# Kernel tuning notes

Hardware: AMD Instinct MI355X
Metric: run time of the kernel (lower is better)

## Reference

```python
import jax, jax.numpy as jnp
import numpy as np

N = 4096          # num_nodes
F = 64            # node_features
H = 128           # hidden_dim
NH = 4            # num_heads
HD = H // NH      # per-head dim = 32
L = 3             # num_layers
C = 7             # num_classes
EDGE_P = 0.004    # ~16 avg degree


def setup_inputs() -> dict:
    key = jax.random.key(0)
    ks = jax.random.split(key, 20)
    g = lambda k, shape, fan_in: jax.random.normal(k, shape, jnp.float32) / np.sqrt(fan_in)
    x = jax.random.normal(ks[0], (N, F), jnp.float32)
    adj = (jax.random.uniform(ks[1], (N, N)) < EDGE_P).astype(jnp.float32)
    return {
        "x": x,
        "adj": adj,
        "enc_W": g(ks[2], (F, H), F), "enc_b": jnp.zeros((H,), jnp.float32),
        "gcn_W": g(ks[3], (L, H, H), H), "gcn_b": jnp.zeros((L, H), jnp.float32),
        "attn_W": g(ks[4], (L, NH, H, HD), H), "attn_Wb": jnp.zeros((L, NH, HD), jnp.float32),
        "attn_a": g(ks[5], (L, NH, 2 * HD), 2 * HD), "attn_ab": jnp.zeros((L, NH), jnp.float32),
        "cls_W1": g(ks[6], (H, H // 2), H), "cls_b1": jnp.zeros((H // 2,), jnp.float32),
        "cls_W2": g(ks[7], (H // 2, C), H // 2), "cls_b2": jnp.zeros((C,), jnp.float32),
        "con_W1": g(ks[8], (H, H // 2), H), "con_b1": jnp.zeros((H // 2,), jnp.float32),
        "con_W2": g(ks[9], (H // 2, 1), H // 2), "con_b2": jnp.zeros((1,), jnp.float32),
    }


def _normalize_adj(adj):
    a = adj + jnp.eye(adj.shape[0], dtype=adj.dtype)
    dinv = jnp.sum(a, axis=1) ** -0.5
    return dinv[:, None] * a * dinv[None, :]


def _gcn(h, adj_norm, W, b):
    support = adj_norm @ h                      # [N,H]
    return jax.nn.relu(support @ W + b)         # dropout=0 (eval)


def _attention(h, edge_mask, W, Wb, a, ab):
    # h:[N,H], W:[NH,H,HD], a:[NH,2*HD]; per-pair score = Linear(concat(h_i,h_j))
    hh = jnp.einsum('nf,hfd->hnd', h, W) + Wb[:, None, :]     # [NH,N,HD]
    a_src, a_dst = a[:, :HD], a[:, HD:]
    s_src = jnp.einsum('hnd,hd->hn', hh, a_src)               # [NH,N]
    s_dst = jnp.einsum('hnd,hd->hn', hh, a_dst)               # [NH,N]
    scores = s_src[:, :, None] + s_dst[:, None, :] + ab[:, None, None]
    # original uses literal 0.0 (NOT -inf) for non-edges before softmax
    scores = jnp.where(edge_mask[None, :, :], scores, 0.0)    # [NH,N,N]
    probs = jax.nn.softmax(scores, axis=-1)
    out = jnp.einsum('hij,hjd->hid', probs, hh)               # [NH,N,HD]
    return out.transpose(1, 0, 2).reshape(h.shape[0], NH * HD)


def reference(x, adj, enc_W, enc_b, gcn_W, gcn_b, attn_W, attn_Wb, attn_a, attn_ab,
              cls_W1, cls_b1, cls_W2, cls_b2, con_W1, con_b1, con_W2, con_b2):
    h = jax.nn.relu(x @ enc_W + enc_b)          # node encoder (dropout=0)
    adj_norm = _normalize_adj(adj)
    edge_mask = adj > 0
    for i in range(L):
        h_gcn = _gcn(h, adj_norm, gcn_W[i], gcn_b[i])
        h_attn = _attention(h, edge_mask, attn_W[i], attn_Wb[i], attn_a[i], attn_ab[i])
        h = jax.nn.relu(h_gcn + h_attn)
    node_logits = jax.nn.relu(h @ cls_W1 + cls_b1) @ cls_W2 + cls_b2
    h_mean = jnp.mean(h, axis=0, keepdims=True)
    contagion = jax.nn.relu(h_mean @ con_W1 + con_b1) @ con_W2 + con_b2
    return (node_logits, h, contagion)
```

## Files before the change

### kernel.cpp

```cpp
#include <hip/hip_runtime.h>

typedef unsigned short u16;
typedef unsigned int u32;

#define N 4096
#define F 64
#define H 128
#define NH 4
#define HD 32
#define EMAX 64

__device__ float g_hA[N * H];
__device__ float g_hB[N * H];
__device__ float g_hhA[N * H];
__device__ float g_hhB[N * H];
__device__ u16   g_cols[N * EMAX];
__device__ int   g_deg[N];
__device__ float g_dinv[N];
__device__ float g_ssrcA[N * NH];
__device__ float g_ssrcB[N * NH];
__device__ float g_sdstA[N * NH];
__device__ float g_sdstB[N * NH];
__device__ float g_part[3][32][H];
__device__ float g_hpart[32][H];

__global__ void k_csr(const float* __restrict__ adj) {
  __shared__ int cnt;
  int row = blockIdx.x;
  if (threadIdx.x == 0) cnt = 0;
  if (row == 0) {
    float* pz = &g_part[0][0][0];
    for (int i = threadIdx.x; i < 3 * 32 * H; i += 256) pz[i] = 0.f;
    float* hz = &g_hpart[0][0];
    for (int i = threadIdx.x; i < 32 * H; i += 256) hz[i] = 0.f;
  }
  __syncthreads();
  int base = threadIdx.x * 16;
  const float4* p = reinterpret_cast<const float4*>(adj + (size_t)row * N + base);
  float4 q0 = p[0], q1 = p[1], q2 = p[2], q3 = p[3];
  float vals[16] = {q0.x, q0.y, q0.z, q0.w, q1.x, q1.y, q1.z, q1.w,
                    q2.x, q2.y, q2.z, q2.w, q3.x, q3.y, q3.z, q3.w};
#pragma unroll
  for (int t = 0; t < 16; ++t)
    if (vals[t] != 0.f) {
      int pos = atomicAdd(&cnt, 1);
      if (pos < EMAX) g_cols[row * EMAX + pos] = (u16)(base + t);
    }
  __syncthreads();
  if (threadIdx.x == 0) {
    g_deg[row] = cnt < EMAX ? cnt : EMAX;
    g_dinv[row] = 1.0f / sqrtf((float)(cnt + 1));
  }
}

__device__ __forceinline__ void agg4(int i0, int tid, const float* __restrict__ h,
                                     const float* __restrict__ hhin,
                                     const float* __restrict__ ssrc_in,
                                     const float* __restrict__ sdst_in,
                                     int l, const float* __restrict__ abv,
                                     int (&jl)[4][EMAX], float (&dv)[4][EMAX],
                                     float (&sdl)[4][EMAX * NH],
                                     float& outa0, float& outa1,
                                     float& sup0, float& sup1) {
  int c = tid & 127, rg = tid >> 7, hc = c >> 5;
  int darr[4];
#pragma unroll
  for (int r = 0; r < 4; ++r) darr[r] = g_deg[i0 + r];
#pragma unroll
  for (int r = 0; r < 4; ++r) {
    const u16* cl = g_cols + (size_t)(i0 + r) * EMAX;
    for (int e = tid; e < darr[r]; e += 256) {
      int j = cl[e];
      jl[r][e] = j;
      dv[r][e] = g_dinv[j];
    }
  }
  __syncthreads();
#pragma unroll
  for (int r = 0; r < 4; ++r)
    for (int idx = tid; idx < darr[r] * NH; idx += 256)
      sdl[r][idx] = sdst_in[jl[r][idx >> 2] * NH + (idx & 3)];
  __syncthreads();

  float sumc = 0.f;
  const float* part = &g_part[l][0][0];
#pragma unroll
  for (int s = 0; s < 32; ++s) sumc += part[s * H + c];
  float ab = abv[hc];

  float oa[2], sp[2];
#pragma unroll
  for (int rr = 0; rr < 2; ++rr) {
    int r = rg * 2 + rr;
    int i = i0 + r, dd = darr[r];
    float ssrc = ssrc_in[i * NH + hc];
    float M = -INFINITY;
    for (int e = 0; e < dd; ++e) M = fmaxf(M, sdl[r][e * NH + hc]);
    float mv = fmaxf(0.f, ssrc + ab + M);
    float em = expf(-mv);
    float base = ssrc + ab - mv;
    float aA = 0.f, aT = 0.f, aG = 0.f, S = 0.f;
    int e = 0;
    for (; e + 2 <= dd; e += 2) {
      int j0 = jl[r][e], j1 = jl[r][e + 1];
      float q0 = hhin[j0 * H + c], q1 = hhin[j1 * H + c];
      float p0 = h[j0 * H + c], p1 = h[j1 * H + c];
      float w0 = expf(base + sdl[r][e * NH + hc]);
      float w1 = expf(base + sdl[r][(e + 1) * NH + hc]);
      aA = fmaf(w0, q0, aA); aA = fmaf(w1, q1, aA);
      aT += q0 + q1;
      aG = fmaf(dv[r][e], p0, aG); aG = fmaf(dv[r][e + 1], p1, aG);
      S += w0 + w1;
    }
    for (; e < dd; ++e) {
      int j = jl[r][e];
      float w = expf(base + sdl[r][e * NH + hc]);
      float q = hhin[j * H + c];
      aA = fmaf(w, q, aA);
      aT += q;
      aG = fmaf(dv[r][e], h[j * H + c], aG);
      S += w;
    }
    float Z = S + em * (float)(N - dd);
    oa[rr] = (aA + em * (sumc - aT)) / Z;
    float di = g_dinv[i];
    sp[rr] = di * (aG + di * h[i * H + c]);
  }
  outa0 = oa[0]; outa1 = oa[1]; sup0 = sp[0]; sup1 = sp[1];
}

__device__ __forceinline__ void proj4(int i0, int tid, const float (&hrowT)[H][4],
                                      const float* __restrict__ aW,
                                      const float* __restrict__ aWb,
                                      const float* __restrict__ aa, int lp,
                                      float* __restrict__ hhout,
                                      float* __restrict__ ssrc_out,
                                      float* __restrict__ sdst_out) {
  int c = tid & 127, rg = tid >> 7, hc = c >> 5, dc = c & 31;
  float b = aWb[hc * HD + dc];
  float p0 = b, p1 = b;
  for (int f = 0; f < H; ++f) {
    float w = aW[(hc * H + f) * HD + dc];
    float2 hv = *reinterpret_cast<const float2*>(&hrowT[f][rg * 2]);
    p0 = fmaf(hv.x, w, p0);
    p1 = fmaf(hv.y, w, p1);
  }
  int r0 = i0 + rg * 2, r1 = r0 + 1;
  hhout[r0 * H + c] = p0;
  hhout[r1 * H + c] = p1;
  const float* ap = aa + hc * 2 * HD;
  float as = ap[dc], ad = ap[HD + dc];
  float ss0 = p0 * as, ss1 = p1 * as, sd0 = p0 * ad, sd1 = p1 * ad;
#pragma unroll
  for (int m = 16; m >= 1; m >>= 1) {
    ss0 += __shfl_xor(ss0, m, 64); ss1 += __shfl_xor(ss1, m, 64);
    sd0 += __shfl_xor(sd0, m, 64); sd1 += __shfl_xor(sd1, m, 64);
  }
  if (dc == 0) {
    ssrc_out[r0 * NH + hc] = ss0; ssrc_out[r1 * NH + hc] = ss1;
    sdst_out[r0 * NH + hc] = sd0; sdst_out[r1 * NH + hc] = sd1;
  }
  atomicAdd(&g_part[lp][r0 & 31][c], p0);
  atomicAdd(&g_part[lp][r1 & 31][c], p1);
}

__global__ void k_enc_proj(const float* __restrict__ x, const float* __restrict__ eW,
                           const float* __restrict__ eb, const float* __restrict__ aW,
                           const float* __restrict__ aWb, const float* __restrict__ aa) {
  __shared__ float xT[F][4];
  __shared__ float hrowT[H][4];
  int i0 = blockIdx.x * 4, tid = threadIdx.x;
  int c = tid & 127, rg = tid >> 7;
  {
    int r = tid >> 6, k = tid & 63;
    xT[k][r] = x[(i0 + r) * F + k];
  }
  __syncthreads();
  float b = eb[c];
  float e0 = b, e1 = b;
  for (int k = 0; k < F; ++k) {
    float w = eW[k * H + c];
    float2 xv = *reinterpret_cast<const float2*>(&xT[k][rg * 2]);
    e0 = fmaf(xv.x, w, e0);
    e1 = fmaf(xv.y, w, e1);
  }
  e0 = fmaxf(e0, 0.f); e1 = fmaxf(e1, 0.f);
  int r0 = i0 + rg * 2, r1 = r0 + 1;
  g_hA[r0 * H + c] = e0; g_hA[r1 * H + c] = e1;
  hrowT[c][rg * 2] = e0; hrowT[c][rg * 2 + 1] = e1;
  __syncthreads();
  proj4(i0, tid, hrowT, aW, aWb, aa, 0, g_hhA, g_ssrcA, g_sdstA);
}

__global__ void k_acp(int pp, int l, const float* __restrict__ gW,
                      const float* __restrict__ gb, const float* __restrict__ aW,
                      const float* __restrict__ aWb, const float* __restrict__ aa,
                      const float* __restrict__ abv) {
  const float* h    = pp ? g_hB : g_hA;
  float*       hout = pp ? g_hA : g_hB;
  const float* hhin = pp ? g_hhB : g_hhA;
  float*       hhout= pp ? g_hhA : g_hhB;
  const float* ssin = pp ? g_ssrcB : g_ssrcA;
  float*       ssout= pp ? g_ssrcA : g_ssrcB;
  const float* sdin = pp ? g_sdstB : g_sdstA;
  float*       sdout= pp ? g_sdstA : g_sdstB;
  __shared__ int   jl[4][EMAX];
  __shared__ float dv[4][EMAX];
  __shared__ float sdl[4][EMAX * NH];
  __shared__ float srowT[H][4];
  __shared__ float hrowT[H][4];
  int i0 = blockIdx.x * 4, tid = threadIdx.x;
  int c = tid & 127, rg = tid >> 7;

  float oa0, oa1, sp0, sp1;
  agg4(i0, tid, h, hhin, ssin, sdin, l, abv, jl, dv, sdl, oa0, oa1, sp0, sp1);
  srowT[c][rg * 2] = sp0; srowT[c][rg * 2 + 1] = sp1;
  __syncthreads();

  float b = gb[c];
  float a0 = b, a1 = b;
  for (int f = 0; f < H; ++f) {
    float w = gW[f * H + c];
    float2 sv = *reinterpret_cast<const float2*>(&srowT[f][rg * 2]);
    a0 = fmaf(sv.x, w, a0);
    a1 = fmaf(sv.y, w, a1);
  }
  float g0 = fmaxf(fmaxf(a0, 0.f) + oa0, 0.f);
  float g1 = fmaxf(fmaxf(a1, 0.f) + oa1, 0.f);
  int r0 = i0 + rg * 2, r1 = r0 + 1;
  hout[r0 * H + c] = g0; hout[r1 * H + c] = g1;
  hrowT[c][rg * 2] = g0; hrowT[c][rg * 2 + 1] = g1;
  __syncthreads();

  proj4(i0, tid, hrowT, aW, aWb, aa, l + 1, hhout, ssout, sdout);
}

__global__ void k_acc(const float* __restrict__ abv, const float* __restrict__ gW,
                      const float* __restrict__ gb,
                      const float* __restrict__ W1, const float* __restrict__ b1,
                      const float* __restrict__ W2, const float* __restrict__ b2,
                      float* __restrict__ out, float* __restrict__ outh) {
  __shared__ int   jl[4][EMAX];
  __shared__ float dv[4][EMAX];
  __shared__ float sdl[4][EMAX * NH];
  __shared__ float srowT[H][4];
  __shared__ float hrowT[H][4];
  __shared__ float tl[4][64];
  int i0 = blockIdx.x * 4, tid = threadIdx.x;
  int c = tid & 127, rg = tid >> 7;

  float oa0, oa1, sp0, sp1;
  agg4(i0, tid, g_hA, g_hhA, g_ssrcA, g_sdstA, 2, abv, jl, dv, sdl, oa0, oa1, sp0, sp1);
  srowT[c][rg * 2] = sp0; srowT[c][rg * 2 + 1] = sp1;
  __syncthreads();

  float b = gb[c];
  float a0 = b, a1 = b;
  for (int f = 0; f < H; ++f) {
    float w = gW[f * H + c];
    float2 sv = *reinterpret_cast<const float2*>(&srowT[f][rg * 2]);
    a0 = fmaf(sv.x, w, a0);
    a1 = fmaf(sv.y, w, a1);
  }
  float g0 = fmaxf(fmaxf(a0, 0.f) + oa0, 0.f);
  float g1 = fmaxf(fmaxf(a1, 0.f) + oa1, 0.f);
  int r0 = i0 + rg * 2, r1 = r0 + 1;
  outh[r0 * H + c] = g0; outh[r1 * H + c] = g1;
  hrowT[c][rg * 2] = g0; hrowT[c][rg * 2 + 1] = g1;
  atomicAdd(&g_hpart[r0 & 31][c], g0);
  atomicAdd(&g_hpart[r1 & 31][c], g1);
  __syncthreads();

  int u = tid & 63, rr4 = tid >> 6;
  float a2 = b1[u];
  for (int f = 0; f < H; ++f) a2 = fmaf(hrowT[f][rr4], W1[f * 64 + u], a2);
  tl[rr4][u] = fmaxf(a2, 0.f);
  __syncthreads();
  if (tid < 28) {
    int r = tid / 7, j = tid - r * 7;
    float p = b2[j];
    for (int v = 0; v < 64; ++v) p = fmaf(tl[r][v], W2[v * 7 + j], p);
    out[(i0 + r) * 7 + j] = p;
  }
}

__global__ void k_contagion(const float* __restrict__ W1, const float* __restrict__ b1,
                            const float* __restrict__ W2, const float* __restrict__ b2,
                            float* __restrict__ out) {
  __shared__ float hm[H];
  __shared__ float tl[64];
  int u = threadIdx.x;
#pragma unroll
  for (int q = 0; q < 2; ++q) {
    int col = u + q * 64;
    float s = 0.f;
#pragma unroll
    for (int sl = 0; sl < 32; ++sl) s += g_hpart[sl][col];
    hm[col] = s * (1.0f / 4096.0f);
  }
  __syncthreads();
  float acc = b1[u];
  for (int f = 0; f < H; ++f) acc = fmaf(hm[f], W1[f * 64 + u], acc);
  tl[u] = fmaxf(acc, 0.f);
  __syncthreads();
  if (u == 0) {
    float p = b2[0];
    for (int v = 0; v < 64; ++v) p = fmaf(tl[v], W2[v], p);
    out[0] = p;
  }
}

extern "C" void kernel_launch(void* const* d_in, const int* in_sizes, int n_in,
                              void* d_out, int out_size, void* d_ws, size_t ws_size,
                              hipStream_t stream) {
  const float* x       = (const float*)d_in[0];
  const float* adj     = (const float*)d_in[1];
  const float* enc_W   = (const float*)d_in[2];
  const float* enc_b   = (const float*)d_in[3];
  const float* gcn_W   = (const float*)d_in[4];
  const float* gcn_b   = (const float*)d_in[5];
  const float* attn_W  = (const float*)d_in[6];
  const float* attn_Wb = (const float*)d_in[7];
  const float* attn_a  = (const float*)d_in[8];
  const float* attn_ab = (const float*)d_in[9];
  const float* cls_W1  = (const float*)d_in[10];
  const float* cls_b1  = (const float*)d_in[11];
  const float* cls_W2  = (const float*)d_in[12];
  const float* cls_b2  = (const float*)d_in[13];
  const float* con_W1  = (const float*)d_in[14];
  const float* con_b1  = (const float*)d_in[15];
  const float* con_W2  = (const float*)d_in[16];
  const float* con_b2  = (const float*)d_in[17];
  (void)in_sizes; (void)n_in; (void)d_ws; (void)ws_size; (void)out_size;

  float* out = (float*)d_out;
  float* outh = out + (size_t)N * 7;
  float* outc = out + (size_t)N * 7 + (size_t)N * H;

  k_csr<<<N, 256, 0, stream>>>(adj);
  k_enc_proj<<<N / 4, 256, 0, stream>>>(x, enc_W, enc_b, attn_W, attn_Wb, attn_a);
  k_acp<<<N / 4, 256, 0, stream>>>(0, 0, gcn_W, gcn_b,
                                   attn_W + (size_t)1 * NH * H * HD,
                                   attn_Wb + (size_t)1 * NH * HD,
                                   attn_a + (size_t)1 * NH * 2 * HD, attn_ab);
  k_acp<<<N / 4, 256, 0, stream>>>(1, 1, gcn_W + (size_t)1 * H * H, gcn_b + H,
                                   attn_W + (size_t)2 * NH * H * HD,
                                   attn_Wb + (size_t)2 * NH * HD,
                                   attn_a + (size_t)2 * NH * 2 * HD, attn_ab + NH);
  k_acc<<<N / 4, 256, 0, stream>>>(attn_ab + 2 * NH, gcn_W + (size_t)2 * H * H,
                                   gcn_b + 2 * H, cls_W1, cls_b1, cls_W2, cls_b2,
                                   out, outh);
  k_contagion<<<1, 64, 0, stream>>>(con_W1, con_b1, con_W2, con_b2, outc);
}
```

Before: 231.8 us.

## Pack h and hh into float2, halve rows per block, fuse CSR build with encoder

Node features h and attention projections hh are interleaved into one float2 array, so each neighbor gather fetches both with a single 8-byte load. Blocks now handle 2 rows instead of 4, doubling the block count. Softmax max, exp weights and their sum are computed once per edge in parallel with wave shuffles and cached in shared memory, rather than recomputed serially per thread. The CSR build and the encoder/projection are merged into one launch, and partial sums are zeroed with a memset. In exchange, weight loads are reused across fewer rows, and the merged kernel runs encoder blocks alongside CSR blocks.

```diff
diff --git a/kernel.cpp b/kernel.cpp
--- a/kernel.cpp
+++ b/kernel.cpp
@@ -1,7 +1,6 @@
 #include <hip/hip_runtime.h>
 
 typedef unsigned short u16;
-typedef unsigned int u32;
 
 #define N 4096
 #define F 64
@@ -9,11 +8,10 @@
 #define NH 4
 #define HD 32
 #define EMAX 64
-
-__device__ float g_hA[N * H];
-__device__ float g_hB[N * H];
-__device__ float g_hhA[N * H];
-__device__ float g_hhB[N * H];
+#define RB 2
+
+__device__ float2 g_pkA[N * H];
+__device__ float2 g_pkB[N * H];
 __device__ u16   g_cols[N * EMAX];
 __device__ int   g_deg[N];
 __device__ float g_dinv[N];
@@ -21,218 +19,206 @@
 __device__ float g_ssrcB[N * NH];
 __device__ float g_sdstA[N * NH];
 __device__ float g_sdstB[N * NH];
-__device__ float g_part[3][32][H];
-__device__ float g_hpart[32][H];
-
-__global__ void k_csr(const float* __restrict__ adj) {
-  __shared__ int cnt;
-  int row = blockIdx.x;
-  if (threadIdx.x == 0) cnt = 0;
-  if (row == 0) {
-    float* pz = &g_part[0][0][0];
-    for (int i = threadIdx.x; i < 3 * 32 * H; i += 256) pz[i] = 0.f;
-    float* hz = &g_hpart[0][0];
-    for (int i = threadIdx.x; i < 32 * H; i += 256) hz[i] = 0.f;
-  }
-  __syncthreads();
-  int base = threadIdx.x * 16;
-  const float4* p = reinterpret_cast<const float4*>(adj + (size_t)row * N + base);
-  float4 q0 = p[0], q1 = p[1], q2 = p[2], q3 = p[3];
-  float vals[16] = {q0.x, q0.y, q0.z, q0.w, q1.x, q1.y, q1.z, q1.w,
-                    q2.x, q2.y, q2.z, q2.w, q3.x, q3.y, q3.z, q3.w};
-#pragma unroll
-  for (int t = 0; t < 16; ++t)
-    if (vals[t] != 0.f) {
-      int pos = atomicAdd(&cnt, 1);
-      if (pos < EMAX) g_cols[row * EMAX + pos] = (u16)(base + t);
-    }
-  __syncthreads();
-  if (threadIdx.x == 0) {
-    g_deg[row] = cnt < EMAX ? cnt : EMAX;
-    g_dinv[row] = 1.0f / sqrtf((float)(cnt + 1));
-  }
-}
-
-__device__ __forceinline__ void agg4(int i0, int tid, const float* __restrict__ h,
-                                     const float* __restrict__ hhin,
+__device__ float g_zr[(3 * 32 + 32) * H];
+
+__device__ __forceinline__ void agg2(int i0, int tid, const float2* __restrict__ pk,
                                      const float* __restrict__ ssrc_in,
                                      const float* __restrict__ sdst_in,
-                                     int l, const float* __restrict__ abv,
-                                     int (&jl)[4][EMAX], float (&dv)[4][EMAX],
-                                     float (&sdl)[4][EMAX * NH],
-                                     float& outa0, float& outa1,
-                                     float& sup0, float& sup1) {
+                                     const float* __restrict__ part,
+                                     const float* __restrict__ abv,
+                                     int (&jl)[RB][EMAX], float (&dv)[RB][EMAX],
+                                     float (&wl)[RB][EMAX * NH],
+                                     float& outa, float& sup) {
   int c = tid & 127, rg = tid >> 7, hc = c >> 5;
-  int darr[4];
-#pragma unroll
-  for (int r = 0; r < 4; ++r) darr[r] = g_deg[i0 + r];
-#pragma unroll
-  for (int r = 0; r < 4; ++r) {
+#pragma unroll
+  for (int r = 0; r < RB; ++r) {
+    int dd = g_deg[i0 + r];
     const u16* cl = g_cols + (size_t)(i0 + r) * EMAX;
-    for (int e = tid; e < darr[r]; e += 256) {
+    for (int e = tid; e < dd; e += 256) {
       int j = cl[e];
       jl[r][e] = j;
       dv[r][e] = g_dinv[j];
     }
   }
   __syncthreads();
-#pragma unroll
-  for (int r = 0; r < 4; ++r)
-    for (int idx = tid; idx < darr[r] * NH; idx += 256)
-      sdl[r][idx] = sdst_in[jl[r][idx >> 2] * NH + (idx & 3)];
+
+  int lg = tid & 31;
+  int i = i0 + rg, dd = g_deg[i];
+  float em, S, base;
+  {
+    float s0 = -INFINITY, s1 = -INFINITY;
+    if (lg < dd)      s0 = sdst_in[jl[rg][lg] * NH + hc];
+    if (lg + 32 < dd) s1 = sdst_in[jl[rg][lg + 32] * NH + hc];
+    float M = fmaxf(s0, s1);
+#pragma unroll
+    for (int m = 16; m >= 1; m >>= 1) M = fmaxf(M, __shfl_xor(M, m, 64));
+    float ssrc = ssrc_in[i * NH + hc];
+    float ab = abv[hc];
+    float mv = fmaxf(0.f, ssrc + ab + M);
+    em = expf(-mv);
+    base = ssrc + ab - mv;
+    float Sp = 0.f;
+    if (lg < dd) {
+      float w0 = expf(base + s0);
+      wl[rg][lg * NH + hc] = w0;
+      Sp = w0;
+    }
+    if (lg + 32 < dd) {
+      float w1 = expf(base + s1);
+      wl[rg][(lg + 32) * NH + hc] = w1;
+      Sp += w1;
+    }
+#pragma unroll
+    for (int m = 16; m >= 1; m >>= 1) Sp += __shfl_xor(Sp, m, 64);
+    S = Sp;
+  }
   __syncthreads();
 
   float sumc = 0.f;
-  const float* part = &g_part[l][0][0];
 #pragma unroll
   for (int s = 0; s < 32; ++s) sumc += part[s * H + c];
-  float ab = abv[hc];
-
-  float oa[2], sp[2];
-#pragma unroll
-  for (int rr = 0; rr < 2; ++rr) {
-    int r = rg * 2 + rr;
-    int i = i0 + r, dd = darr[r];
-    float ssrc = ssrc_in[i * NH + hc];
-    float M = -INFINITY;
-    for (int e = 0; e < dd; ++e) M = fmaxf(M, sdl[r][e * NH + hc]);
-    float mv = fmaxf(0.f, ssrc + ab + M);
-    float em = expf(-mv);
-    float base = ssrc + ab - mv;
-    float aA = 0.f, aT = 0.f, aG = 0.f, S = 0.f;
-    int e = 0;
-    for (; e + 2 <= dd; e += 2) {
-      int j0 = jl[r][e], j1 = jl[r][e + 1];
-      float q0 = hhin[j0 * H + c], q1 = hhin[j1 * H + c];
-      float p0 = h[j0 * H + c], p1 = h[j1 * H + c];
-      float w0 = expf(base + sdl[r][e * NH + hc]);
-      float w1 = expf(base + sdl[r][(e + 1) * NH + hc]);
-      aA = fmaf(w0, q0, aA); aA = fmaf(w1, q1, aA);
-      aT += q0 + q1;
-      aG = fmaf(dv[r][e], p0, aG); aG = fmaf(dv[r][e + 1], p1, aG);
-      S += w0 + w1;
-    }
-    for (; e < dd; ++e) {
-      int j = jl[r][e];
-      float w = expf(base + sdl[r][e * NH + hc]);
-      float q = hhin[j * H + c];
-      aA = fmaf(w, q, aA);
-      aT += q;
-      aG = fmaf(dv[r][e], h[j * H + c], aG);
-      S += w;
-    }
-    float Z = S + em * (float)(N - dd);
-    oa[rr] = (aA + em * (sumc - aT)) / Z;
-    float di = g_dinv[i];
-    sp[rr] = di * (aG + di * h[i * H + c]);
-  }
-  outa0 = oa[0]; outa1 = oa[1]; sup0 = sp[0]; sup1 = sp[1];
-}
-
-__device__ __forceinline__ void proj4(int i0, int tid, const float (&hrowT)[H][4],
+
+  const float2* pkc = pk + c;
+  float aA = 0.f, aT = 0.f, aG = 0.f;
+  int e = 0;
+  for (; e + 4 <= dd; e += 4) {
+    int j0 = jl[rg][e],     j1 = jl[rg][e + 1];
+    int j2 = jl[rg][e + 2], j3 = jl[rg][e + 3];
+    float2 q0 = pkc[j0 * H], q1 = pkc[j1 * H];
+    float2 q2 = pkc[j2 * H], q3 = pkc[j3 * H];
+    float w0 = wl[rg][e * NH + hc],       w1 = wl[rg][(e + 1) * NH + hc];
+    float w2 = wl[rg][(e + 2) * NH + hc], w3 = wl[rg][(e + 3) * NH + hc];
+    aA = fmaf(w0, q0.y, aA); aA = fmaf(w1, q1.y, aA);
+    aA = fmaf(w2, q2.y, aA); aA = fmaf(w3, q3.y, aA);
+    aT += (q0.y + q1.y) + (q2.y + q3.y);
+    aG = fmaf(dv[rg][e], q0.x, aG);     aG = fmaf(dv[rg][e + 1], q1.x, aG);
+    aG = fmaf(dv[rg][e + 2], q2.x, aG); aG = fmaf(dv[rg][e + 3], q3.x, aG);
+  }
+  for (; e < dd; ++e) {
+    int j = jl[rg][e];
+    float2 q = pkc[j * H];
+    float w = wl[rg][e * NH + hc];
+    aA = fmaf(w, q.y, aA);
+    aT += q.y;
+    aG = fmaf(dv[rg][e], q.x, aG);
+  }
+  float Z = S + em * (float)(N - dd);
+  outa = (aA + em * (sumc - aT)) / Z;
+  float di = g_dinv[i];
+  sup = di * (aG + di * pkc[i * H].x);
+}
+
+__device__ __forceinline__ void proj2(int i0, int tid, const float (&hrowT)[H][RB],
                                       const float* __restrict__ aW,
                                       const float* __restrict__ aWb,
-                                      const float* __restrict__ aa, int lp,
-                                      float* __restrict__ hhout,
+                                      const float* __restrict__ aa,
+                                      float* __restrict__ part, float hval,
+                                      float2* __restrict__ pkout,
                                       float* __restrict__ ssrc_out,
                                       float* __restrict__ sdst_out) {
   int c = tid & 127, rg = tid >> 7, hc = c >> 5, dc = c & 31;
-  float b = aWb[hc * HD + dc];
-  float p0 = b, p1 = b;
-  for (int f = 0; f < H; ++f) {
-    float w = aW[(hc * H + f) * HD + dc];
-    float2 hv = *reinterpret_cast<const float2*>(&hrowT[f][rg * 2]);
-    p0 = fmaf(hv.x, w, p0);
-    p1 = fmaf(hv.y, w, p1);
-  }
-  int r0 = i0 + rg * 2, r1 = r0 + 1;
-  hhout[r0 * H + c] = p0;
-  hhout[r1 * H + c] = p1;
+  float p = aWb[hc * HD + dc];
+  for (int f = 0; f < H; ++f)
+    p = fmaf(hrowT[f][rg], aW[(hc * H + f) * HD + dc], p);
+  int r = i0 + rg;
+  pkout[r * H + c] = make_float2(hval, p);
   const float* ap = aa + hc * 2 * HD;
-  float as = ap[dc], ad = ap[HD + dc];
-  float ss0 = p0 * as, ss1 = p1 * as, sd0 = p0 * ad, sd1 = p1 * ad;
+  float ss = p * ap[dc], sd = p * ap[HD + dc];
 #pragma unroll
   for (int m = 16; m >= 1; m >>= 1) {
-    ss0 += __shfl_xor(ss0, m, 64); ss1 += __shfl_xor(ss1, m, 64);
-    sd0 += __shfl_xor(sd0, m, 64); sd1 += __shfl_xor(sd1, m, 64);
+    ss += __shfl_xor(ss, m, 64);
+    sd += __shfl_xor(sd, m, 64);
   }
   if (dc == 0) {
-    ssrc_out[r0 * NH + hc] = ss0; ssrc_out[r1 * NH + hc] = ss1;
-    sdst_out[r0 * NH + hc] = sd0; sdst_out[r1 * NH + hc] = sd1;
-  }
-  atomicAdd(&g_part[lp][r0 & 31][c], p0);
-  atomicAdd(&g_part[lp][r1 & 31][c], p1);
-}
-
-__global__ void k_enc_proj(const float* __restrict__ x, const float* __restrict__ eW,
-                           const float* __restrict__ eb, const float* __restrict__ aW,
-                           const float* __restrict__ aWb, const float* __restrict__ aa) {
-  __shared__ float xT[F][4];
-  __shared__ float hrowT[H][4];
-  int i0 = blockIdx.x * 4, tid = threadIdx.x;
-  int c = tid & 127, rg = tid >> 7;
-  {
-    int r = tid >> 6, k = tid & 63;
-    xT[k][r] = x[(i0 + r) * F + k];
-  }
-  __syncthreads();
-  float b = eb[c];
-  float e0 = b, e1 = b;
-  for (int k = 0; k < F; ++k) {
-    float w = eW[k * H + c];
-    float2 xv = *reinterpret_cast<const float2*>(&xT[k][rg * 2]);
-    e0 = fmaf(xv.x, w, e0);
-    e1 = fmaf(xv.y, w, e1);
-  }
-  e0 = fmaxf(e0, 0.f); e1 = fmaxf(e1, 0.f);
-  int r0 = i0 + rg * 2, r1 = r0 + 1;
-  g_hA[r0 * H + c] = e0; g_hA[r1 * H + c] = e1;
-  hrowT[c][rg * 2] = e0; hrowT[c][rg * 2 + 1] = e1;
-  __syncthreads();
-  proj4(i0, tid, hrowT, aW, aWb, aa, 0, g_hhA, g_ssrcA, g_sdstA);
+    ssrc_out[r * NH + hc] = ss;
+    sdst_out[r * NH + hc] = sd;
+  }
+  atomicAdd(&part[(r & 31) * H + c], p);
+}
+
+__global__ void k_csr_enc(const float* __restrict__ adj, const float* __restrict__ x,
+                          const float* __restrict__ eW, const float* __restrict__ eb,
+                          const float* __restrict__ aW, const float* __restrict__ aWb,
+                          const float* __restrict__ aa) {
+  __shared__ float xT[F][RB];
+  __shared__ float hrowT[H][RB];
+  __shared__ int cnt;
+  int tid = threadIdx.x;
+  if (blockIdx.x < N / RB) {
+    int i0 = blockIdx.x * RB;
+    int c = tid & 127, rg = tid >> 7;
+    if (tid < F * RB) {
+      int r = tid >> 6, k = tid & 63;
+      xT[k][r] = x[(i0 + r) * F + k];
+    }
+    __syncthreads();
+    float e = eb[c];
+    for (int k = 0; k < F; ++k)
+      e = fmaf(xT[k][rg], eW[k * H + c], e);
+    e = fmaxf(e, 0.f);
+    hrowT[c][rg] = e;
+    __syncthreads();
+    proj2(i0, tid, hrowT, aW, aWb, aa, g_zr, e, g_pkA, g_ssrcA, g_sdstA);
+  } else {
+    int row = blockIdx.x - N / RB;
+    if (tid == 0) cnt = 0;
+    __syncthreads();
+    const float* rp = adj + (size_t)row * N;
+    float4 q[4];
+#pragma unroll
+    for (int k2 = 0; k2 < 4; ++k2)
+      q[k2] = *reinterpret_cast<const float4*>(rp + k2 * 1024 + tid * 4);
+#pragma unroll
+    for (int k2 = 0; k2 < 4; ++k2) {
+      int base = k2 * 1024 + tid * 4;
+      float v[4] = {q[k2].x, q[k2].y, q[k2].z, q[k2].w};
+#pragma unroll
+      for (int t = 0; t < 4; ++t)
+        if (v[t] != 0.f) {
+          int pos = atomicAdd(&cnt, 1);
+          if (pos < EMAX) g_cols[row * EMAX + pos] = (u16)(base + t);
+        }
+    }
+    __syncthreads();
+    if (tid == 0) {
+      g_deg[row] = cnt < EMAX ? cnt : EMAX;
+      g_dinv[row] = 1.0f / sqrtf((float)(cnt + 1));
+    }
+  }
 }
 
 __global__ void k_acp(int pp, int l, const float* __restrict__ gW,
                       const float* __restrict__ gb, const float* __restrict__ aW,
                       const float* __restrict__ aWb, const float* __restrict__ aa,
                       const float* __restrict__ abv) {
-  const float* h    = pp ? g_hB : g_hA;
-  float*       hout = pp ? g_hA : g_hB;
-  const float* hhin = pp ? g_hhB : g_hhA;
-  float*       hhout= pp ? g_hhA : g_hhB;
-  const float* ssin = pp ? g_ssrcB : g_ssrcA;
-  float*       ssout= pp ? g_ssrcA : g_ssrcB;
-  const float* sdin = pp ? g_sdstB : g_sdstA;
-  float*       sdout= pp ? g_sdstA : g_sdstB;
-  __shared__ int   jl[4][EMAX];
-  __shared__ float dv[4][EMAX];
-  __shared__ float sdl[4][EMAX * NH];
-  __shared__ float srowT[H][4];
-  __shared__ float hrowT[H][4];
-  int i0 = blockIdx.x * 4, tid = threadIdx.x;
+  const float2* pk    = pp ? g_pkB : g_pkA;
+  float2*       pkout = pp ? g_pkA : g_pkB;
+  const float*  ssin  = pp ? g_ssrcB : g_ssrcA;
+  float*        ssout = pp ? g_ssrcA : g_ssrcB;
+  const float*  sdin  = pp ? g_sdstB : g_sdstA;
+  float*        sdout = pp ? g_sdstA : g_sdstB;
+  __shared__ int   jl[RB][EMAX];
+  __shared__ float dv[RB][EMAX];
+  __shared__ float wl[RB][EMAX * NH];
+  __shared__ float srowT[H][RB];
+  __shared__ float hrowT[H][RB];
+  int i0 = blockIdx.x * RB, tid = threadIdx.x;
   int c = tid & 127, rg = tid >> 7;
 
-  float oa0, oa1, sp0, sp1;
-  agg4(i0, tid, h, hhin, ssin, sdin, l, abv, jl, dv, sdl, oa0, oa1, sp0, sp1);
-  srowT[c][rg * 2] = sp0; srowT[c][rg * 2 + 1] = sp1;
-  __syncthreads();
-
-  float b = gb[c];
-  float a0 = b, a1 = b;
-  for (int f = 0; f < H; ++f) {
-    float w = gW[f * H + c];
-    float2 sv = *reinterpret_cast<const float2*>(&srowT[f][rg * 2]);
-    a0 = fmaf(sv.x, w, a0);
-    a1 = fmaf(sv.y, w, a1);
-  }
-  float g0 = fmaxf(fmaxf(a0, 0.f) + oa0, 0.f);
-  float g1 = fmaxf(fmaxf(a1, 0.f) + oa1, 0.f);
-  int r0 = i0 + rg * 2, r1 = r0 + 1;
-  hout[r0 * H + c] = g0; hout[r1 * H + c] = g1;
-  hrowT[c][rg * 2] = g0; hrowT[c][rg * 2 + 1] = g1;
-  __syncthreads();
-
-  proj4(i0, tid, hrowT, aW, aWb, aa, l + 1, hhout, ssout, sdout);
+  float oa, sp;
+  agg2(i0, tid, pk, ssin, sdin, g_zr + l * 32 * H, abv, jl, dv, wl, oa, sp);
+  srowT[c][rg] = sp;
+  __syncthreads();
+
+  float a = gb[c];
+  for (int f = 0; f < H; ++f)
+    a = fmaf(srowT[f][rg], gW[f * H + c], a);
+  float g = fmaxf(fmaxf(a, 0.f) + oa, 0.f);
+  hrowT[c][rg] = g;
+  __syncthreads();
+
+  proj2(i0, tid, hrowT, aW, aWb, aa, g_zr + (l + 1) * 32 * H, g,
+        pkout, ssout, sdout);
 }
 
 __global__ void k_acc(const float* __restrict__ abv, const float* __restrict__ gW,
@@ -240,47 +226,44 @@
                       const float* __restrict__ W1, const float* __restrict__ b1,
                       const float* __restrict__ W2, const float* __restrict__ b2,
                       float* __restrict__ out, float* __restrict__ outh) {
-  __shared__ int   jl[4][EMAX];
-  __shared__ float dv[4][EMAX];
-  __shared__ float sdl[4][EMAX * NH];
-  __shared__ float srowT[H][4];
-  __shared__ float hrowT[H][4];
-  __shared__ float tl[4][64];
-  int i0 = blockIdx.x * 4, tid = threadIdx.x;
+  __shared__ int   jl[RB][EMAX];
+  __shared__ float dv[RB][EMAX];
+  __shared__ float wl[RB][EMAX * NH];
+  __shared__ float srowT[H][RB];
+  __shared__ float hrowT[H][RB];
+  __shared__ float tl[RB][64];
+  int i0 = blockIdx.x * RB, tid = threadIdx.x;
   int c = tid & 127, rg = tid >> 7;
 
-  float oa0, oa1, sp0, sp1;
-  agg4(i0, tid, g_hA, g_hhA, g_ssrcA, g_sdstA, 2, abv, jl, dv, sdl, oa0, oa1, sp0, sp1);
-  srowT[c][rg * 2] = sp0; srowT[c][rg * 2 + 1] = sp1;
-  __syncthreads();
-
-  float b = gb[c];
-  float a0 = b, a1 = b;
-  for (int f = 0; f < H; ++f) {
-    float w = gW[f * H + c];
-    float2 sv = *reinterpret_cast<const float2*>(&srowT[f][rg * 2]);
-    a0 = fmaf(sv.x, w, a0);
-    a1 = fmaf(sv.y, w, a1);
-  }
-  float g0 = fmaxf(fmaxf(a0, 0.f) + oa0, 0.f);
-  float g1 = fmaxf(fmaxf(a1, 0.f) + oa1, 0.f);
-  int r0 = i0 + rg * 2, r1 = r0 + 1;
-  outh[r0 * H + c] = g0; outh[r1 * H + c] = g1;
-  hrowT[c][rg * 2] = g0; hrowT[c][rg * 2 + 1] = g1;
-  atomicAdd(&g_hpart[r0 & 31][c], g0);
-  atomicAdd(&g_hpart[r1 & 31][c], g1);
-  __syncthreads();
-
-  int u = tid & 63, rr4 = tid >> 6;
-  float a2 = b1[u];
-  for (int f = 0; f < H; ++f) a2 = fmaf(hrowT[f][rr4], W1[f * 64 + u], a2);
-  tl[rr4][u] = fmaxf(a2, 0.f);
-  __syncthreads();
-  if (tid < 28) {
-    int r = tid / 7, j = tid - r * 7;
+  float oa, sp;
+  agg2(i0, tid, g_pkA, g_ssrcA, g_sdstA, g_zr + 2 * 32 * H, abv, jl, dv, wl, oa, sp);
+  srowT[c][rg] = sp;
+  __syncthreads();
+
+  float a = gb[c];
+  for (int f = 0; f < H; ++f)
+    a = fmaf(srowT[f][rg], gW[f * H + c], a);
+  float g = fmaxf(fmaxf(a, 0.f) + oa, 0.f);
+  int r = i0 + rg;
+  outh[r * H + c] = g;
+  hrowT[c][rg] = g;
+  atomicAdd(&g_zr[(3 * 32 + (r & 31)) * H + c], g);
+  __syncthreads();
+
+  if (tid < 128) {
+    int rr = tid >> 6, u = tid & 63;
+    float a2 = b1[u];
+    for (int f = 0; f < H; ++f)
+      a2 = fmaf(hrowT[f][rr], W1[f * 64 + u], a2);
+    tl[rr][u] = fmaxf(a2, 0.f);
+  }
+  __syncthreads();
+  if (tid < 7 * RB) {
+    int rr = tid / 7, j = tid - rr * 7;
     float p = b2[j];
-    for (int v = 0; v < 64; ++v) p = fmaf(tl[r][v], W2[v * 7 + j], p);
-    out[(i0 + r) * 7 + j] = p;
+    for (int v = 0; v < 64; ++v)
+      p = fmaf(tl[rr][v], W2[v * 7 + j], p);
+    out[(i0 + rr) * 7 + j] = p;
   }
 }
 
@@ -290,12 +273,13 @@
   __shared__ float hm[H];
   __shared__ float tl[64];
   int u = threadIdx.x;
+  const float* hp = g_zr + 3 * 32 * H;
 #pragma unroll
   for (int q = 0; q < 2; ++q) {
     int col = u + q * 64;
     float s = 0.f;
 #pragma unroll
-    for (int sl = 0; sl < 32; ++sl) s += g_hpart[sl][col];
+    for (int sl = 0; sl < 32; ++sl) s += hp[sl * H + col];
     hm[col] = s * (1.0f / 4096.0f);
   }
   __syncthreads();
@@ -337,18 +321,22 @@
   float* outh = out + (size_t)N * 7;
   float* outc = out + (size_t)N * 7 + (size_t)N * H;
 
-  k_csr<<<N, 256, 0, stream>>>(adj);
-  k_enc_proj<<<N / 4, 256, 0, stream>>>(x, enc_W, enc_b, attn_W, attn_Wb, attn_a);
-  k_acp<<<N / 4, 256, 0, stream>>>(0, 0, gcn_W, gcn_b,
-                                   attn_W + (size_t)1 * NH * H * HD,
-                                   attn_Wb + (size_t)1 * NH * HD,
-                                   attn_a + (size_t)1 * NH * 2 * HD, attn_ab);
-  k_acp<<<N / 4, 256, 0, stream>>>(1, 1, gcn_W + (size_t)1 * H * H, gcn_b + H,
-                                   attn_W + (size_t)2 * NH * H * HD,
-                                   attn_Wb + (size_t)2 * NH * HD,
-                                   attn_a + (size_t)2 * NH * 2 * HD, attn_ab + NH);
-  k_acc<<<N / 4, 256, 0, stream>>>(attn_ab + 2 * NH, gcn_W + (size_t)2 * H * H,
-                                   gcn_b + 2 * H, cls_W1, cls_b1, cls_W2, cls_b2,
-                                   out, outh);
+  void* zr = nullptr;
+  hipGetSymbolAddress(&zr, HIP_SYMBOL(g_zr));
+  hipMemsetAsync(zr, 0, sizeof(float) * (3 * 32 + 32) * H, stream);
+
+  k_csr_enc<<<N / RB + N, 256, 0, stream>>>(adj, x, enc_W, enc_b,
+                                            attn_W, attn_Wb, attn_a);
+  k_acp<<<N / RB, 256, 0, stream>>>(0, 0, gcn_W, gcn_b,
+                                    attn_W + (size_t)1 * NH * H * HD,
+                                    attn_Wb + (size_t)1 * NH * HD,
+                                    attn_a + (size_t)1 * NH * 2 * HD, attn_ab);
+  k_acp<<<N / RB, 256, 0, stream>>>(1, 1, gcn_W + (size_t)1 * H * H, gcn_b + H,
+                                    attn_W + (size_t)2 * NH * H * HD,
+                                    attn_Wb + (size_t)2 * NH * HD,
+                                    attn_a + (size_t)2 * NH * 2 * HD, attn_ab + NH);
+  k_acc<<<N / RB, 256, 0, stream>>>(attn_ab + 2 * NH, gcn_W + (size_t)2 * H * H,
+                                    gcn_b + 2 * H, cls_W1, cls_b1, cls_W2, cls_b2,
+                                    out, outh);
   k_contagion<<<1, 64, 0, stream>>>(con_W1, con_b1, con_W2, con_b2, outc);
 }
```

Result: slower. 244.4 us (+5.4%).
